# Performance work log

Hardware: AMD Instinct MI355X
Metric: run time of the kernel (lower is better)

## Reference

```python
import jax, jax.numpy as jnp
import numpy as np

D_MODEL = 256
N_LEVELS = 4
N_HEADS = 8
N_POINTS = 4
D_HEAD = D_MODEL // N_HEADS
SPATIAL = np.array([[32, 64, 64], [16, 32, 32], [8, 16, 16], [4, 8, 8]], dtype=np.int32)  # (D,H,W) per level


def _offset_bias():
    # replicates _reset_parameters grid_init for sampling_offsets.bias
    thetas = np.arange(N_HEADS, dtype=np.float64) * (2.0 * np.pi / N_HEADS)
    phis = np.tile(np.array([np.pi / 4, -np.pi / 4]), (N_HEADS + 1) // 2)[:N_HEADS]
    dirs = np.stack([np.cos(thetas) * np.cos(phis), np.sin(thetas) * np.cos(phis), np.sin(phis)], axis=-1)  # (H,3)
    scales = (np.arange(N_POINTS) + 1.0) / (N_POINTS + 1.0)  # (P,)
    grid = np.broadcast_to(dirs[:, None, None, :], (N_HEADS, N_LEVELS, N_POINTS, 3)) * scales[None, None, :, None]
    return jnp.asarray(grid.reshape(-1), jnp.float32)


def setup_inputs() -> dict:
    key = jax.random.key(0)
    ks = jax.random.split(key, 8)
    N, Lq = 2, 8192
    Len_in = int(SPATIAL.prod(axis=1).sum())
    starts = np.concatenate([[0], np.cumsum(SPATIAL.prod(axis=1))[:-1]]).astype(np.int32)
    s = 1.0 / np.sqrt(D_MODEL)
    return {
        "query": jax.random.normal(ks[0], (N, Lq, D_MODEL), jnp.float32),
        "reference_points": jax.random.uniform(ks[1], (N, Lq, N_LEVELS, 3), jnp.float32),
        "input_flatten": jax.random.normal(ks[2], (N, Len_in, D_MODEL), jnp.float32),
        "input_spatial_shapes": jnp.asarray(SPATIAL),
        "input_level_start_index": jnp.asarray(starts),
        "Wv": jax.random.normal(ks[3], (D_MODEL, D_MODEL), jnp.float32) * s,
        "bv": jnp.zeros((D_MODEL,), jnp.float32),
        "Woff": jax.random.normal(ks[4], (D_MODEL, N_HEADS * N_LEVELS * N_POINTS * 3), jnp.float32) * 0.02,
        "boff": _offset_bias(),
        "Wattn": jax.random.normal(ks[5], (D_MODEL, N_HEADS * N_LEVELS * N_POINTS), jnp.float32) * s,
        "battn": jnp.zeros((N_HEADS * N_LEVELS * N_POINTS,), jnp.float32),
        "Wout": jax.random.normal(ks[6], (D_MODEL, D_MODEL), jnp.float32) * s,
        "bout": jnp.zeros((D_MODEL,), jnp.float32),
    }


def _sample_level(vl, loc, D, H, W):
    # vl: (N, D*H*W, Hd, c) flat per-level value; loc: (N, Lq, Hd, P, 3) normalized (x,y,z) in [0,1]
    # grid_sample semantics, align_corners=False, zero padding
    N, Hd = vl.shape[0], vl.shape[2]
    x = loc[..., 0] * W - 0.5
    y = loc[..., 1] * H - 0.5
    z = loc[..., 2] * D - 0.5
    x0 = jnp.floor(x); y0 = jnp.floor(y); z0 = jnp.floor(z)
    fx = x - x0; fy = y - y0; fz = z - z0
    x0i = x0.astype(jnp.int32); y0i = y0.astype(jnp.int32); z0i = z0.astype(jnp.int32)
    bidx = jnp.arange(N)[:, None, None, None]
    hidx = jnp.arange(Hd)[None, None, :, None]

    def corner(xi, yi, zi, w):
        valid = (xi >= 0) & (xi < W) & (yi >= 0) & (yi < H) & (zi >= 0) & (zi < D)
        idx = (jnp.clip(zi, 0, D - 1) * H + jnp.clip(yi, 0, H - 1)) * W + jnp.clip(xi, 0, W - 1)
        g = vl[bidx, idx, hidx]  # (N, Lq, Hd, P, c)
        return g * (w * valid)[..., None]

    return (corner(x0i,     y0i,     z0i,     (1 - fx) * (1 - fy) * (1 - fz))
          + corner(x0i + 1, y0i,     z0i,     fx       * (1 - fy) * (1 - fz))
          + corner(x0i,     y0i + 1, z0i,     (1 - fx) * fy       * (1 - fz))
          + corner(x0i + 1, y0i + 1, z0i,     fx       * fy       * (1 - fz))
          + corner(x0i,     y0i,     z0i + 1, (1 - fx) * (1 - fy) * fz)
          + corner(x0i + 1, y0i,     z0i + 1, fx       * (1 - fy) * fz)
          + corner(x0i,     y0i + 1, z0i + 1, (1 - fx) * fy       * fz)
          + corner(x0i + 1, y0i + 1, z0i + 1, fx       * fy       * fz))


def reference(query, reference_points, input_flatten, input_spatial_shapes, input_level_start_index,
              Wv, bv, Woff, boff, Wattn, battn, Wout, bout):
    shapes = np.asarray(input_spatial_shapes)          # static (L,3): (D,H,W)
    starts = np.asarray(input_level_start_index)       # static (L,)
    N, Lq, _ = query.shape
    value = (input_flatten @ Wv + bv).reshape(N, -1, N_HEADS, D_HEAD)
    off = (query @ Woff + boff).reshape(N, Lq, N_HEADS, N_LEVELS, N_POINTS, 3)
    attn = jax.nn.softmax((query @ Wattn + battn).reshape(N, Lq, N_HEADS, N_LEVELS * N_POINTS), axis=-1)
    attn = attn.reshape(N, Lq, N_HEADS, N_LEVELS, N_POINTS)
    # offset normalizer: (W,H,D) per level -> (x,y,z) order
    norm = jnp.asarray(shapes[:, [2, 1, 0]], jnp.float32)  # (L,3)
    loc = reference_points[:, :, None, :, None, :] + off / norm[None, None, None, :, None, :]
    out = jnp.zeros((N, Lq, N_HEADS, D_HEAD), query.dtype)
    for l in range(N_LEVELS):
        D, H, W = int(shapes[l, 0]), int(shapes[l, 1]), int(shapes[l, 2])
        vl = value[:, int(starts[l]):int(starts[l]) + D * H * W]
        sampled = _sample_level(vl, loc[:, :, :, l], D, H, W)  # (N,Lq,Hd,P,c)
        out = out + jnp.einsum('nqhpc,nqhp->nqhc', sampled, attn[:, :, :, l])
    return out.reshape(N, Lq, D_MODEL) @ Wout + bout
```

## Files before the change

kernel.cpp:

```cpp
#include <hip/hip_runtime.h>
#include <hip/hip_bf16.h>

#define NBATCH   2
#define LQ       8192
#define DMODEL   256
#define NHEADS   8
#define DHEAD    32
#define NLEVELS  4
#define NPOINTS  4
#define LEN_IN   149760
#define QB       8

using short8 = __attribute__((ext_vector_type(8))) short;
using f32x4v = __attribute__((ext_vector_type(4))) float;

__device__ __forceinline__ int iclamp(int v, int lo, int hi) {
    return v < lo ? lo : (v > hi ? hi : v);
}

__device__ __forceinline__ f32x4v mfma_bf16_16x16x32(short8 a, short8 b, f32x4v c) {
    asm volatile("v_mfma_f32_16x16x32_bf16 %0, %1, %2, %0"
                 : "+v"(c) : "v"(a), "v"(b));
    return c;
}

__global__ __launch_bounds__(256) void wsplit_kernel(
    const float* __restrict__ W, short* __restrict__ WhT, short* __restrict__ WlT)
{
    const int n = blockIdx.x;
    const int k = threadIdx.x;
    const float w = W[k * 256 + n];
    __hip_bfloat16 h = __float2bfloat16(w);
    const float hf = __bfloat162float(h);
    __hip_bfloat16 l = __float2bfloat16(w - hf);
    WhT[n * 256 + k] = *reinterpret_cast<unsigned short*>(&h);
    WlT[n * 256 + k] = *reinterpret_cast<unsigned short*>(&l);
}

__global__ __launch_bounds__(256, 2) void gemm3t_kernel(
    const float* __restrict__ A, const short* __restrict__ BhT,
    const short* __restrict__ BlT, const float* __restrict__ bias,
    float* __restrict__ Y)
{
    __shared__ short Ah[128][64], Al[128][64], Bh[128][64], Bl[128][64];
    const int tid  = threadIdx.x;
    const int lane = tid & 63;
    const int wv   = tid >> 6;
    const int wrow = wv >> 1, wcol = wv & 1;
    const int l16  = lane & 15, lkg = lane >> 4;
    const size_t row0 = (size_t)blockIdx.x * 128;
    const int    col0 = blockIdx.y * 128;

    f32x4v acc[4][4];
    #pragma unroll
    for (int m = 0; m < 4; ++m)
        #pragma unroll
        for (int n = 0; n < 4; ++n) acc[m][n] = (f32x4v){0.f, 0.f, 0.f, 0.f};

    for (int k0 = 0; k0 < 256; k0 += 64) {
        __syncthreads();
        #pragma unroll
        for (int i = 0; i < 4; ++i) {
            const int s = i * 256 + tid;
            const int r = s >> 3, k8 = s & 7;
            const float* g = A + (row0 + r) * 256 + k0 + k8 * 8;
            const float4 a0 = *(const float4*)g;
            const float4 a1 = *(const float4*)(g + 4);
            const float av[8] = {a0.x, a0.y, a0.z, a0.w, a1.x, a1.y, a1.z, a1.w};
            short hi[8], lo[8];
            #pragma unroll
            for (int j = 0; j < 8; ++j) {
                __hip_bfloat16 h = __float2bfloat16(av[j]);
                const float hf = __bfloat162float(h);
                __hip_bfloat16 l = __float2bfloat16(av[j] - hf);
                hi[j] = *reinterpret_cast<unsigned short*>(&h);
                lo[j] = *reinterpret_cast<unsigned short*>(&l);
            }
            const int p = k8 ^ (r & 7);
            *(short8*)&Ah[r][p * 8] = *(const short8*)hi;
            *(short8*)&Al[r][p * 8] = *(const short8*)lo;
        }
        #pragma unroll
        for (int i = 0; i < 4; ++i) {
            const int s = i * 256 + tid;
            const int r = s >> 3, k8 = s & 7;
            const int p = k8 ^ (r & 7);
            const size_t go = (size_t)(col0 + r) * 256 + k0 + k8 * 8;
            *(short8*)&Bh[r][p * 8] = *(const short8*)(BhT + go);
            *(short8*)&Bl[r][p * 8] = *(const short8*)(BlT + go);
        }
        __syncthreads();
        #pragma unroll
        for (int kk = 0; kk < 2; ++kk) {
            const int slot = kk * 4 + lkg;
            short8 ah[4], al[4], bh[4], bl[4];
            #pragma unroll
            for (int m = 0; m < 4; ++m) {
                const int r = wrow * 64 + m * 16 + l16;
                const int p = slot ^ (r & 7);
                ah[m] = *(const short8*)&Ah[r][p * 8];
                al[m] = *(const short8*)&Al[r][p * 8];
            }
            #pragma unroll
            for (int n = 0; n < 4; ++n) {
                const int r = wcol * 64 + n * 16 + l16;
                const int p = slot ^ (r & 7);
                bh[n] = *(const short8*)&Bh[r][p * 8];
                bl[n] = *(const short8*)&Bl[r][p * 8];
            }
            #pragma unroll
            for (int m = 0; m < 4; ++m)
                #pragma unroll
                for (int n = 0; n < 4; ++n) {
                    acc[m][n] = mfma_bf16_16x16x32(ah[m], bh[n], acc[m][n]);
                    acc[m][n] = mfma_bf16_16x16x32(ah[m], bl[n], acc[m][n]);
                    acc[m][n] = mfma_bf16_16x16x32(al[m], bh[n], acc[m][n]);
                }
        }
    }
    asm volatile("s_nop 7\n\ts_nop 7\n\ts_nop 7" ::: );
    #pragma unroll
    for (int n = 0; n < 4; ++n) {
        const int col = col0 + wcol * 64 + n * 16 + l16;
        const float b = bias[col];
        #pragma unroll
        for (int m = 0; m < 4; ++m) {
            const size_t row = row0 + wrow * 64 + m * 16 + lkg * 4;
            #pragma unroll
            for (int r = 0; r < 4; ++r)
                Y[(row + r) * 256 + col] = acc[m][n][r] + b;
        }
    }
}

__global__ __launch_bounds__(256) void deform_kernel(
    const float* __restrict__ query, const float* __restrict__ refp,
    const float* __restrict__ value, const int* __restrict__ shapes,
    const int* __restrict__ starts, const float* __restrict__ Woff,
    const float* __restrict__ boff, const float* __restrict__ Wattn,
    const float* __restrict__ battn, float* __restrict__ mid)
{
    __shared__ float q_lds[QB][256];
    __shared__ float off_lds[QB][384];
    __shared__ float attn_lds[QB][128];
    __shared__ float rp_lds[QB][12];
    __shared__ int   shp_s[12];
    __shared__ int   st_s[4];

    const int tid = threadIdx.x;
    const size_t gq0 = (size_t)blockIdx.x * QB;

    {
        const float4* Qv = (const float4*)(query + gq0 * 256);
        float4* Qs = (float4*)q_lds;
        Qs[tid]       = Qv[tid];
        Qs[tid + 256] = Qv[tid + 256];
    }
    if (tid < QB * 12) ((float*)rp_lds)[tid] = refp[gq0 * 12 + tid];
    if (tid < 12) shp_s[tid] = shapes[tid];
    if (tid < 4)  st_s[tid]  = starts[tid];
    __syncthreads();

    {
        float acc0[QB], acc1[QB];
        #pragma unroll
        for (int q = 0; q < QB; ++q) { acc0[q] = 0.f; acc1[q] = 0.f; }
        const bool lo = (tid < 128);
        for (int k = 0; k < 256; k += 4) {
            float w0[4], w1[4];
            #pragma unroll
            for (int kk = 0; kk < 4; ++kk) {
                w0[kk] = Woff[(size_t)(k + kk) * 384 + tid];
                w1[kk] = lo ? Woff[(size_t)(k + kk) * 384 + 256 + tid]
                            : Wattn[(size_t)(k + kk) * 128 + (tid - 128)];
            }
            #pragma unroll
            for (int q = 0; q < QB; ++q) {
                const float4 a4 = *(const float4*)&q_lds[q][k];
                acc0[q] = fmaf(a4.x, w0[0], acc0[q]);
                acc0[q] = fmaf(a4.y, w0[1], acc0[q]);
                acc0[q] = fmaf(a4.z, w0[2], acc0[q]);
                acc0[q] = fmaf(a4.w, w0[3], acc0[q]);
                acc1[q] = fmaf(a4.x, w1[0], acc1[q]);
                acc1[q] = fmaf(a4.y, w1[1], acc1[q]);
                acc1[q] = fmaf(a4.z, w1[2], acc1[q]);
                acc1[q] = fmaf(a4.w, w1[3], acc1[q]);
            }
        }
        const float b0 = boff[tid];
        const float b1 = lo ? boff[256 + tid] : battn[tid - 128];
        #pragma unroll
        for (int q = 0; q < QB; ++q) {
            off_lds[q][tid] = acc0[q] + b0;
            if (lo) off_lds[q][256 + tid]  = acc1[q] + b1;
            else    attn_lds[q][tid - 128] = acc1[q] + b1;
        }
    }
    __syncthreads();

    if (tid < QB * NHEADS) {
        const int q = tid >> 3, h = tid & 7;
        float* lg = &attn_lds[q][h * 16];
        float m = lg[0];
        #pragma unroll
        for (int j = 1; j < 16; ++j) m = fmaxf(m, lg[j]);
        float s = 0.f;
        #pragma unroll
        for (int j = 0; j < 16; ++j) { const float e = __expf(lg[j] - m); lg[j] = e; s += e; }
        const float inv = 1.f / s;
        #pragma unroll
        for (int j = 0; j < 16; ++j) lg[j] *= inv;
    }
    __syncthreads();

    const int lane   = tid & 63;
    const int wv     = tid >> 6;
    const int corner = lane >> 3;
    const int dxl = corner & 1, dyl = (corner >> 1) & 1, dzl = (corner >> 2) & 1;
    const int c4  = lane & 7;

    for (int pp = wv; pp < QB * NHEADS; pp += 4) {
        const int q = pp >> 3, h = pp & 7;
        const size_t gq = gq0 + (size_t)q;
        const int b = (int)(gq >> 13);
        float4 acc = {0.f, 0.f, 0.f, 0.f};
        #pragma unroll
        for (int l = 0; l < NLEVELS; ++l) {
            const int Dd = shp_s[l * 3 + 0], Hh = shp_s[l * 3 + 1], Ww = shp_s[l * 3 + 2];
            const float fD = (float)Dd, fH = (float)Hh, fW = (float)Ww;
            const float* vbase = value + ((size_t)b * LEN_IN + st_s[l]) * 256 + h * 32 + c4 * 4;
            const float rx = rp_lds[q][l * 3 + 0];
            const float ry = rp_lds[q][l * 3 + 1];
            const float rz = rp_lds[q][l * 3 + 2];
            #pragma unroll
            for (int p = 0; p < NPOINTS; ++p) {
                const int oidx = ((h * 4 + l) * 4 + p) * 3;
                const float x = fmaf(rx, fW, off_lds[q][oidx + 0]) - 0.5f;
                const float y = fmaf(ry, fH, off_lds[q][oidx + 1]) - 0.5f;
                const float z = fmaf(rz, fD, off_lds[q][oidx + 2]) - 0.5f;
                const float aw = attn_lds[q][(h * 4 + l) * 4 + p];
                const float xf = floorf(x), yf = floorf(y), zf = floorf(z);
                const float fx = x - xf, fy = y - yf, fz = z - zf;
                const int xi = (int)xf + dxl, yi = (int)yf + dyl, zi = (int)zf + dzl;
                const float wx = dxl ? fx : 1.f - fx;
                const float wy = dyl ? fy : 1.f - fy;
                const float wz = dzl ? fz : 1.f - fz;
                const bool valid = (xi >= 0) & (xi < Ww) & (yi >= 0) & (yi < Hh) &
                                   (zi >= 0) & (zi < Dd);
                const int xc = iclamp(xi, 0, Ww - 1);
                const int yc = iclamp(yi, 0, Hh - 1);
                const int zc = iclamp(zi, 0, Dd - 1);
                const float wgt = valid ? (aw * wx * wy * wz) : 0.f;
                const float4 v = *(const float4*)(vbase + (size_t)((zc * Hh + yc) * Ww + xc) * 256);
                acc.x = fmaf(wgt, v.x, acc.x);
                acc.y = fmaf(wgt, v.y, acc.y);
                acc.z = fmaf(wgt, v.z, acc.z);
                acc.w = fmaf(wgt, v.w, acc.w);
            }
        }
        #pragma unroll
        for (int m = 8; m <= 32; m <<= 1) {
            acc.x += __shfl_xor(acc.x, m);
            acc.y += __shfl_xor(acc.y, m);
            acc.z += __shfl_xor(acc.z, m);
            acc.w += __shfl_xor(acc.w, m);
        }
        if (corner == 0)
            *(float4*)&mid[gq * 256 + h * 32 + c4 * 4] = acc;
    }
}

extern "C" void kernel_launch(void* const* d_in, const int* in_sizes, int n_in,
                              void* d_out, int out_size, void* d_ws, size_t ws_size,
                              hipStream_t stream) {
    const float* query  = (const float*)d_in[0];
    const float* refp   = (const float*)d_in[1];
    const float* xin    = (const float*)d_in[2];
    const int*   shapes = (const int*)d_in[3];
    const int*   starts = (const int*)d_in[4];
    const float* Wv     = (const float*)d_in[5];
    const float* bv     = (const float*)d_in[6];
    const float* Woff   = (const float*)d_in[7];
    const float* boff   = (const float*)d_in[8];
    const float* Wattn  = (const float*)d_in[9];
    const float* battn  = (const float*)d_in[10];
    const float* Wout   = (const float*)d_in[11];
    const float* bout   = (const float*)d_in[12];
    float* out = (float*)d_out;

    float* value = (float*)d_ws;
    float* mid   = value + (size_t)NBATCH * LEN_IN * 256;
    short* WvhT  = (short*)(mid + (size_t)NBATCH * LQ * 256);
    short* WvlT  = WvhT + 256 * 256;
    short* WohT  = WvlT + 256 * 256;
    short* WolT  = WohT + 256 * 256;

    const int vrows = NBATCH * LEN_IN;
    const int qrows = NBATCH * LQ;

    wsplit_kernel<<<256, 256, 0, stream>>>(Wv, WvhT, WvlT);
    wsplit_kernel<<<256, 256, 0, stream>>>(Wout, WohT, WolT);
    gemm3t_kernel<<<dim3(vrows / 128, 2), 256, 0, stream>>>(xin, WvhT, WvlT, bv, value);
    deform_kernel<<<qrows / QB, 256, 0, stream>>>(query, refp, value, shapes, starts,
                                                  Woff, boff, Wattn, battn, mid);
    gemm3t_kernel<<<dim3(qrows / 128, 2), 256, 0, stream>>>(mid, WohT, WolT, bout, out);
}
```

Before: 830.8 us.

## Move offset/attention projection to MFMA GEMM, restructure deform sampling, prefetch GEMM tiles

Computes the sampling-offset and attention-logit projections with the split-bf16 MFMA GEMM into a workspace buffer, replacing the scalar FMA projection inside the deform kernel. The deform kernel is rewritten so each lane computes one corner/point descriptor (index and trilinear weight) and distributes it via ds_bpermute. Spatial shapes and level starts are hardcoded rather than read from inputs, and the softmax normalisation is applied after the reduction. The GEMM also gains register prefetch of the next K tile. This adds an extra 16K×512 round trip through global memory and hardcodes level geometry.

```diff
diff --git a/kernel.cpp b/kernel.cpp
--- a/kernel.cpp
+++ b/kernel.cpp
@@ -5,11 +5,9 @@
 #define LQ       8192
 #define DMODEL   256
 #define NHEADS   8
-#define DHEAD    32
 #define NLEVELS  4
 #define NPOINTS  4
 #define LEN_IN   149760
-#define QB       8
 
 using short8 = __attribute__((ext_vector_type(8))) short;
 using f32x4v = __attribute__((ext_vector_type(4))) float;
@@ -37,10 +35,26 @@
     WlT[n * 256 + k] = *reinterpret_cast<unsigned short*>(&l);
 }
 
+__global__ __launch_bounds__(256) void wsplit_proj_kernel(
+    const float* __restrict__ Woff, const float* __restrict__ Wattn,
+    const float* __restrict__ boff, const float* __restrict__ battn,
+    short* __restrict__ WhT, short* __restrict__ WlT, float* __restrict__ bp)
+{
+    const int n = blockIdx.x;
+    const int k = threadIdx.x;
+    const float w = (n < 384) ? Woff[k * 384 + n] : Wattn[k * 128 + (n - 384)];
+    __hip_bfloat16 h = __float2bfloat16(w);
+    const float hf = __bfloat162float(h);
+    __hip_bfloat16 l = __float2bfloat16(w - hf);
+    WhT[n * 256 + k] = *reinterpret_cast<unsigned short*>(&h);
+    WlT[n * 256 + k] = *reinterpret_cast<unsigned short*>(&l);
+    if (k == 0) bp[n] = (n < 384) ? boff[n] : battn[n - 384];
+}
+
 __global__ __launch_bounds__(256, 2) void gemm3t_kernel(
     const float* __restrict__ A, const short* __restrict__ BhT,
     const short* __restrict__ BlT, const float* __restrict__ bias,
-    float* __restrict__ Y)
+    float* __restrict__ Y, const int ldy)
 {
     __shared__ short Ah[128][64], Al[128][64], Bh[128][64], Bl[128][64];
     const int tid  = threadIdx.x;
@@ -57,16 +71,32 @@
         #pragma unroll
         for (int n = 0; n < 4; ++n) acc[m][n] = (f32x4v){0.f, 0.f, 0.f, 0.f};
 
-    for (int k0 = 0; k0 < 256; k0 += 64) {
+    float4 pa0[4], pa1[4];
+    short8 pbh[4], pbl[4];
+
+    auto load_tile = [&](int k0) {
+        #pragma unroll
+        for (int i = 0; i < 4; ++i) {
+            const int sl = i * 256 + tid;
+            const int r = sl >> 3, k8 = sl & 7;
+            const float* g = A + (row0 + r) * 256 + k0 + k8 * 8;
+            pa0[i] = *(const float4*)g;
+            pa1[i] = *(const float4*)(g + 4);
+            const size_t go = (size_t)(col0 + r) * 256 + k0 + k8 * 8;
+            pbh[i] = *(const short8*)(BhT + go);
+            pbl[i] = *(const short8*)(BlT + go);
+        }
+    };
+
+    load_tile(0);
+    for (int t = 0; t < 4; ++t) {
         __syncthreads();
         #pragma unroll
         for (int i = 0; i < 4; ++i) {
-            const int s = i * 256 + tid;
-            const int r = s >> 3, k8 = s & 7;
-            const float* g = A + (row0 + r) * 256 + k0 + k8 * 8;
-            const float4 a0 = *(const float4*)g;
-            const float4 a1 = *(const float4*)(g + 4);
-            const float av[8] = {a0.x, a0.y, a0.z, a0.w, a1.x, a1.y, a1.z, a1.w};
+            const int sl = i * 256 + tid;
+            const int r = sl >> 3, k8 = sl & 7;
+            const float av[8] = {pa0[i].x, pa0[i].y, pa0[i].z, pa0[i].w,
+                                 pa1[i].x, pa1[i].y, pa1[i].z, pa1[i].w};
             short hi[8], lo[8];
             #pragma unroll
             for (int j = 0; j < 8; ++j) {
@@ -79,17 +109,11 @@
             const int p = k8 ^ (r & 7);
             *(short8*)&Ah[r][p * 8] = *(const short8*)hi;
             *(short8*)&Al[r][p * 8] = *(const short8*)lo;
-        }
-        #pragma unroll
-        for (int i = 0; i < 4; ++i) {
-            const int s = i * 256 + tid;
-            const int r = s >> 3, k8 = s & 7;
-            const int p = k8 ^ (r & 7);
-            const size_t go = (size_t)(col0 + r) * 256 + k0 + k8 * 8;
-            *(short8*)&Bh[r][p * 8] = *(const short8*)(BhT + go);
-            *(short8*)&Bl[r][p * 8] = *(const short8*)(BlT + go);
+            *(short8*)&Bh[r][p * 8] = pbh[i];
+            *(short8*)&Bl[r][p * 8] = pbl[i];
         }
         __syncthreads();
+        if (t < 3) load_tile((t + 1) * 64);
         #pragma unroll
         for (int kk = 0; kk < 2; ++kk) {
             const int slot = kk * 4 + lkg;
@@ -128,145 +152,118 @@
             const size_t row = row0 + wrow * 64 + m * 16 + lkg * 4;
             #pragma unroll
             for (int r = 0; r < 4; ++r)
-                Y[(row + r) * 256 + col] = acc[m][n][r] + b;
+                Y[(row + r) * (size_t)ldy + col] = acc[m][n][r] + b;
         }
     }
 }
 
-__global__ __launch_bounds__(256) void deform_kernel(
-    const float* __restrict__ query, const float* __restrict__ refp,
-    const float* __restrict__ value, const int* __restrict__ shapes,
-    const int* __restrict__ starts, const float* __restrict__ Woff,
-    const float* __restrict__ boff, const float* __restrict__ Wattn,
-    const float* __restrict__ battn, float* __restrict__ mid)
-{
-    __shared__ float q_lds[QB][256];
-    __shared__ float off_lds[QB][384];
-    __shared__ float attn_lds[QB][128];
-    __shared__ float rp_lds[QB][12];
-    __shared__ int   shp_s[12];
-    __shared__ int   st_s[4];
-
-    const int tid = threadIdx.x;
-    const size_t gq0 = (size_t)blockIdx.x * QB;
-
-    {
-        const float4* Qv = (const float4*)(query + gq0 * 256);
-        float4* Qs = (float4*)q_lds;
-        Qs[tid]       = Qv[tid];
-        Qs[tid + 256] = Qv[tid + 256];
-    }
-    if (tid < QB * 12) ((float*)rp_lds)[tid] = refp[gq0 * 12 + tid];
-    if (tid < 12) shp_s[tid] = shapes[tid];
-    if (tid < 4)  st_s[tid]  = starts[tid];
-    __syncthreads();
-
-    {
-        float acc0[QB], acc1[QB];
-        #pragma unroll
-        for (int q = 0; q < QB; ++q) { acc0[q] = 0.f; acc1[q] = 0.f; }
-        const bool lo = (tid < 128);
-        for (int k = 0; k < 256; k += 4) {
-            float w0[4], w1[4];
-            #pragma unroll
-            for (int kk = 0; kk < 4; ++kk) {
-                w0[kk] = Woff[(size_t)(k + kk) * 384 + tid];
-                w1[kk] = lo ? Woff[(size_t)(k + kk) * 384 + 256 + tid]
-                            : Wattn[(size_t)(k + kk) * 128 + (tid - 128)];
-            }
-            #pragma unroll
-            for (int q = 0; q < QB; ++q) {
-                const float4 a4 = *(const float4*)&q_lds[q][k];
-                acc0[q] = fmaf(a4.x, w0[0], acc0[q]);
-                acc0[q] = fmaf(a4.y, w0[1], acc0[q]);
-                acc0[q] = fmaf(a4.z, w0[2], acc0[q]);
-                acc0[q] = fmaf(a4.w, w0[3], acc0[q]);
-                acc1[q] = fmaf(a4.x, w1[0], acc1[q]);
-                acc1[q] = fmaf(a4.y, w1[1], acc1[q]);
-                acc1[q] = fmaf(a4.z, w1[2], acc1[q]);
-                acc1[q] = fmaf(a4.w, w1[3], acc1[q]);
-            }
-        }
-        const float b0 = boff[tid];
-        const float b1 = lo ? boff[256 + tid] : battn[tid - 128];
-        #pragma unroll
-        for (int q = 0; q < QB; ++q) {
-            off_lds[q][tid] = acc0[q] + b0;
-            if (lo) off_lds[q][256 + tid]  = acc1[q] + b1;
-            else    attn_lds[q][tid - 128] = acc1[q] + b1;
-        }
-    }
-    __syncthreads();
-
-    if (tid < QB * NHEADS) {
-        const int q = tid >> 3, h = tid & 7;
-        float* lg = &attn_lds[q][h * 16];
-        float m = lg[0];
-        #pragma unroll
-        for (int j = 1; j < 16; ++j) m = fmaxf(m, lg[j]);
-        float s = 0.f;
-        #pragma unroll
-        for (int j = 0; j < 16; ++j) { const float e = __expf(lg[j] - m); lg[j] = e; s += e; }
-        const float inv = 1.f / s;
-        #pragma unroll
-        for (int j = 0; j < 16; ++j) lg[j] *= inv;
-    }
-    __syncthreads();
-
+__device__ __forceinline__ int2 geom_desc(int d, int q, int b, int h,
+        const float* __restrict__ proj, const float* __restrict__ refp)
+{
+    const int pi = d >> 3;
+    const int cn = d & 7;
+    const int l  = pi >> 2;
+    const int ws_ = 6 - l;
+    const int W  = 1 << ws_;
+    const int Dd = W >> 1;
+    const float fW = (float)W, fD = (float)Dd;
+    const int cx = cn & 1, cy = (cn >> 1) & 1, cz = cn >> 2;
+    const size_t prow = (size_t)q * 512;
+    const float ox = proj[prow + h * 48 + pi * 3 + 0];
+    const float oy = proj[prow + h * 48 + pi * 3 + 1];
+    const float oz = proj[prow + h * 48 + pi * 3 + 2];
+    const int rb = q * 12 + l * 3;
+    const float rx = refp[rb + 0], ry = refp[rb + 1], rz = refp[rb + 2];
+    const float x = fmaf(rx, fW, ox) - 0.5f;
+    const float y = fmaf(ry, fW, oy) - 0.5f;
+    const float z = fmaf(rz, fD, oz) - 0.5f;
+    const float xf = floorf(x), yf = floorf(y), zf = floorf(z);
+    const float fx = x - xf, fy = y - yf, fz = z - zf;
+    const int x0 = (int)xf + cx, y0 = (int)yf + cy, z0 = (int)zf + cz;
+    const float wx = cx ? fx : 1.f - fx;
+    const float wy = cy ? fy : 1.f - fy;
+    const float wz = cz ? fz : 1.f - fz;
+    const bool valid = ((unsigned)x0 < (unsigned)W) & ((unsigned)y0 < (unsigned)W) &
+                       ((unsigned)z0 < (unsigned)Dd);
+    const int xc = iclamp(x0, 0, W - 1);
+    const int yc = iclamp(y0, 0, W - 1);
+    const int zc = iclamp(z0, 0, Dd - 1);
+    const int voxel = (((zc << ws_) + yc) << ws_) + xc;
+    const int start = 0x24800 & (int)(0xFFFFFFFFu << (18 - 3 * l));
+    const int idx = ((b ? LEN_IN : 0) + start + voxel) << 8;
+    const float w3 = valid ? wx * wy * wz : 0.f;
+    return make_int2(idx, __float_as_int(w3));
+}
+
+__global__ __launch_bounds__(256, 8) void deform_kernel(
+    const float* __restrict__ refp, const float* __restrict__ value,
+    const float* __restrict__ proj, float* __restrict__ mid)
+{
+    const int tid    = threadIdx.x;
     const int lane   = tid & 63;
     const int wv     = tid >> 6;
     const int corner = lane >> 3;
-    const int dxl = corner & 1, dyl = (corner >> 1) & 1, dzl = (corner >> 2) & 1;
-    const int c4  = lane & 7;
-
-    for (int pp = wv; pp < QB * NHEADS; pp += 4) {
-        const int q = pp >> 3, h = pp & 7;
-        const size_t gq = gq0 + (size_t)q;
-        const int b = (int)(gq >> 13);
+    const int c4     = lane & 7;
+    const int wid    = blockIdx.x * 4 + wv;
+    const int pair0  = wid * 16;
+
+    #pragma unroll 1
+    for (int i16 = 0; i16 < 16; ++i16) {
+        const int pair = pair0 + i16;
+        const int q = pair >> 3;
+        const int h = pair & 7;
+        const int b = q >> 13;
+        const float* lg = proj + (size_t)q * 512 + 384 + h * 16;
+        const float4 L0 = *(const float4*)(lg + 0);
+        const float4 L1 = *(const float4*)(lg + 4);
+        const float4 L2 = *(const float4*)(lg + 8);
+        const float4 L3 = *(const float4*)(lg + 12);
+        float m = fmaxf(fmaxf(fmaxf(L0.x, L0.y), fmaxf(L0.z, L0.w)),
+                        fmaxf(fmaxf(L1.x, L1.y), fmaxf(L1.z, L1.w)));
+        m = fmaxf(m, fmaxf(fmaxf(fmaxf(L2.x, L2.y), fmaxf(L2.z, L2.w)),
+                           fmaxf(fmaxf(L3.x, L3.y), fmaxf(L3.z, L3.w))));
+        float e[16];
+        e[0] = __expf(L0.x - m);  e[1] = __expf(L0.y - m);
+        e[2] = __expf(L0.z - m);  e[3] = __expf(L0.w - m);
+        e[4] = __expf(L1.x - m);  e[5] = __expf(L1.y - m);
+        e[6] = __expf(L1.z - m);  e[7] = __expf(L1.w - m);
+        e[8] = __expf(L2.x - m);  e[9] = __expf(L2.y - m);
+        e[10] = __expf(L2.z - m); e[11] = __expf(L2.w - m);
+        e[12] = __expf(L3.x - m); e[13] = __expf(L3.y - m);
+        e[14] = __expf(L3.z - m); e[15] = __expf(L3.w - m);
+        float s = 0.f;
+        #pragma unroll
+        for (int j = 0; j < 16; ++j) s += e[j];
+        const float inv = 1.f / s;
+        const int2 d0 = geom_desc(lane, q, b, h, proj, refp);
+        const int2 d1 = geom_desc(lane + 64, q, b, h, proj, refp);
+        const int hoff = h * 32 + c4 * 4;
         float4 acc = {0.f, 0.f, 0.f, 0.f};
         #pragma unroll
-        for (int l = 0; l < NLEVELS; ++l) {
-            const int Dd = shp_s[l * 3 + 0], Hh = shp_s[l * 3 + 1], Ww = shp_s[l * 3 + 2];
-            const float fD = (float)Dd, fH = (float)Hh, fW = (float)Ww;
-            const float* vbase = value + ((size_t)b * LEN_IN + st_s[l]) * 256 + h * 32 + c4 * 4;
-            const float rx = rp_lds[q][l * 3 + 0];
-            const float ry = rp_lds[q][l * 3 + 1];
-            const float rz = rp_lds[q][l * 3 + 2];
-            #pragma unroll
-            for (int p = 0; p < NPOINTS; ++p) {
-                const int oidx = ((h * 4 + l) * 4 + p) * 3;
-                const float x = fmaf(rx, fW, off_lds[q][oidx + 0]) - 0.5f;
-                const float y = fmaf(ry, fH, off_lds[q][oidx + 1]) - 0.5f;
-                const float z = fmaf(rz, fD, off_lds[q][oidx + 2]) - 0.5f;
-                const float aw = attn_lds[q][(h * 4 + l) * 4 + p];
-                const float xf = floorf(x), yf = floorf(y), zf = floorf(z);
-                const float fx = x - xf, fy = y - yf, fz = z - zf;
-                const int xi = (int)xf + dxl, yi = (int)yf + dyl, zi = (int)zf + dzl;
-                const float wx = dxl ? fx : 1.f - fx;
-                const float wy = dyl ? fy : 1.f - fy;
-                const float wz = dzl ? fz : 1.f - fz;
-                const bool valid = (xi >= 0) & (xi < Ww) & (yi >= 0) & (yi < Hh) &
-                                   (zi >= 0) & (zi < Dd);
-                const int xc = iclamp(xi, 0, Ww - 1);
-                const int yc = iclamp(yi, 0, Hh - 1);
-                const int zc = iclamp(zi, 0, Dd - 1);
-                const float wgt = valid ? (aw * wx * wy * wz) : 0.f;
-                const float4 v = *(const float4*)(vbase + (size_t)((zc * Hh + yc) * Ww + xc) * 256);
-                acc.x = fmaf(wgt, v.x, acc.x);
-                acc.y = fmaf(wgt, v.y, acc.y);
-                acc.z = fmaf(wgt, v.z, acc.z);
-                acc.w = fmaf(wgt, v.w, acc.w);
-            }
-        }
-        #pragma unroll
-        for (int m = 8; m <= 32; m <<= 1) {
-            acc.x += __shfl_xor(acc.x, m);
-            acc.y += __shfl_xor(acc.y, m);
-            acc.z += __shfl_xor(acc.z, m);
-            acc.w += __shfl_xor(acc.w, m);
-        }
-        if (corner == 0)
-            *(float4*)&mid[gq * 256 + h * 32 + c4 * 4] = acc;
+        for (int p = 0; p < 16; ++p) {
+            const int sa = ((p & 7) * 8 + corner) * 4;
+            const int rawi = (p < 8) ? d0.x : d1.x;
+            const int raww = (p < 8) ? d0.y : d1.y;
+            const int idx   = __builtin_amdgcn_ds_bpermute(sa, rawi);
+            const int wbits = __builtin_amdgcn_ds_bpermute(sa, raww);
+            const float wgt = __int_as_float(wbits) * e[p];
+            const float4 v = *(const float4*)(value + (size_t)(unsigned)idx + hoff);
+            acc.x = fmaf(wgt, v.x, acc.x);
+            acc.y = fmaf(wgt, v.y, acc.y);
+            acc.z = fmaf(wgt, v.z, acc.z);
+            acc.w = fmaf(wgt, v.w, acc.w);
+        }
+        #pragma unroll
+        for (int mm = 8; mm <= 32; mm <<= 1) {
+            acc.x += __shfl_xor(acc.x, mm);
+            acc.y += __shfl_xor(acc.y, mm);
+            acc.z += __shfl_xor(acc.z, mm);
+            acc.w += __shfl_xor(acc.w, mm);
+        }
+        if (corner == 0) {
+            acc.x *= inv; acc.y *= inv; acc.z *= inv; acc.w *= inv;
+            *(float4*)&mid[(size_t)q * 256 + hoff] = acc;
+        }
     }
 }
 
@@ -276,8 +273,6 @@
     const float* query  = (const float*)d_in[0];
     const float* refp   = (const float*)d_in[1];
     const float* xin    = (const float*)d_in[2];
-    const int*   shapes = (const int*)d_in[3];
-    const int*   starts = (const int*)d_in[4];
     const float* Wv     = (const float*)d_in[5];
     const float* bv     = (const float*)d_in[6];
     const float* Woff   = (const float*)d_in[7];
@@ -290,18 +285,27 @@
 
     float* value = (float*)d_ws;
     float* mid   = value + (size_t)NBATCH * LEN_IN * 256;
-    short* WvhT  = (short*)(mid + (size_t)NBATCH * LQ * 256);
+    float* proj  = mid + (size_t)NBATCH * LQ * 256;
+    short* WvhT  = (short*)(proj + (size_t)NBATCH * LQ * 512);
     short* WvlT  = WvhT + 256 * 256;
     short* WohT  = WvlT + 256 * 256;
     short* WolT  = WohT + 256 * 256;
+    short* WphT  = WolT + 256 * 256;
+    short* WplT  = WphT + 512 * 256;
+    float* bp    = (float*)(WplT + 512 * 256);
 
     const int vrows = NBATCH * LEN_IN;
     const int qrows = NBATCH * LQ;
 
     wsplit_kernel<<<256, 256, 0, stream>>>(Wv, WvhT, WvlT);
     wsplit_kernel<<<256, 256, 0, stream>>>(Wout, WohT, WolT);
-    gemm3t_kernel<<<dim3(vrows / 128, 2), 256, 0, stream>>>(xin, WvhT, WvlT, bv, value);
-    deform_kernel<<<qrows / QB, 256, 0, stream>>>(query, refp, value, shapes, starts,
-                                                  Woff, boff, Wattn, battn, mid);
-    gemm3t_kernel<<<dim3(qrows / 128, 2), 256, 0, stream>>>(mid, WohT, WolT, bout, out);
-}
+    wsplit_proj_kernel<<<512, 256, 0, stream>>>(Woff, Wattn, boff, battn,
+                                                WphT, WplT, bp);
+    gemm3t_kernel<<<dim3(qrows / 128, 4), 256, 0, stream>>>(query, WphT, WplT, bp,
+                                                            proj, 512);
+    gemm3t_kernel<<<dim3(vrows / 128, 2), 256, 0, stream>>>(xin, WvhT, WvlT, bv,
+                                                            value, 256);
+    deform_kernel<<<2048, 256, 0, stream>>>(refp, value, proj, mid);
+    gemm3t_kernel<<<dim3(qrows / 128, 2), 256, 0, stream>>>(mid, WohT, WolT, bout,
+                                                            out, 256);
+}
```

Result: faster. 778.1 us (-6.3%).
